# Kernel tuning notes

Measured on AMD Instinct MI355X. Metric: run time of the kernel, lower is better.

## Reference

```python
import jax, jax.numpy as jnp
import numpy as np

N = 1024      # num_waves
L = 32        # latent_dim
H = 64        # hidden_dim
EPS = 1e-6
SELF_SCALE = 0.5
INT_SCALE = 0.3


def _xavier(k, shape, gain=0.5):
    fan_out, fan_in = shape
    std = gain * np.sqrt(2.0 / (fan_in + fan_out))
    return (jax.random.normal(k, shape, jnp.float32) * std).astype(jnp.float32)


def setup_inputs() -> dict:
    key = jax.random.key(0)
    ks = jax.random.split(key, 12)
    d = {}
    d['state'] = jax.random.normal(ks[0], (N * (L + 1),), jnp.float32)
    # SelfDynamicsNetwork: L->H->H->L, tanh, xavier_normal gain=0.5, zero bias
    d['Ws1'] = _xavier(ks[1], (H, L)); d['bs1'] = jnp.zeros((H,), jnp.float32)
    d['Ws2'] = _xavier(ks[2], (H, H)); d['bs2'] = jnp.zeros((H,), jnp.float32)
    d['Ws3'] = _xavier(ks[3], (L, H)); d['bs3'] = jnp.zeros((L,), jnp.float32)
    # InteractionNetwork: 4L->H->H->L
    d['Wi1'] = _xavier(ks[4], (H, 4 * L)); d['bi1'] = jnp.zeros((H,), jnp.float32)
    d['Wi2'] = _xavier(ks[5], (H, H));     d['bi2'] = jnp.zeros((H,), jnp.float32)
    d['Wi3'] = _xavier(ks[6], (L, H));     d['bi3'] = jnp.zeros((L,), jnp.float32)
    # QuantumPhaseMixer
    d['phase_w'] = jax.random.normal(ks[7], (L,), jnp.float32) * 0.1
    d['Wc'] = _xavier(ks[8], (L, 2 * L), gain=1.0)
    d['bc'] = jnp.zeros((L,), jnp.float32)
    # per-wave aggressiveness
    d['aggr'] = jnp.ones((N,), jnp.float32) * 0.5
    return d


def reference(state, Ws1, bs1, Ws2, bs2, Ws3, bs3,
              Wi1, bi1, Wi2, bi2, Wi3, bi3,
              phase_w, Wc, bc, aggr):
    s = state.reshape(N, L + 1)
    h = s[:, :L]          # [N, L]
    phases = s[:, L]      # [N]

    def mlp(x, W1, b1, W2, b2, W3, b3):
        x = jnp.tanh(x @ W1.T + b1)
        x = jnp.tanh(x @ W2.T + b2)
        return x @ W3.T + b3

    self_term = mlp(h, Ws1, bs1, Ws2, bs2, Ws3, bs3)   # [N, L]
    dh = self_term  # prev_state is None -> estimated velocity = self_dynamics(h)

    # pairwise distance factor
    diff = h[:, None, :] - h[None, :, :]                # [N, N, L] (h_i - h_j)
    dist = jnp.linalg.norm(diff, axis=-1) + EPS         # [N, N]
    dfac = jnp.minimum(1.0 / dist, 2.0)

    # InteractionNetwork on concat([h_i, h_j, dh_i, dh_j]): split first layer
    a_i = h @ Wi1[:, :L].T + dh @ Wi1[:, 2 * L:3 * L].T           # [N, H]
    b_j = h @ Wi1[:, L:2 * L].T + dh @ Wi1[:, 3 * L:].T + bi1    # [N, H]
    x1 = jnp.tanh(a_i[:, None, :] + b_j[None, :, :])              # [N, N, H]
    x2 = jnp.tanh(x1 @ Wi2.T + bi2)                               # [N, N, H]
    k_ij = x2 @ Wi3.T + bi3                                       # [N, N, L]

    # QuantumPhaseMixer
    phase_diff = phases[:, None] - phases[None, :]                # [N, N]
    pf = jnp.cos(phase_diff[..., None] * phase_w)                 # [N, N, L]
    coh = jax.nn.sigmoid((h @ Wc[:, :L].T)[:, None, :]
                         + (h @ Wc[:, L:].T)[None, :, :] + bc)    # [N, N, L]
    quantum = pf * coh * (-diff)                                  # h_j - h_i = -diff

    agg = jax.nn.sigmoid(aggr)                                    # [N]
    inter = dfac[..., None] * k_ij * agg[:, None, None] + quantum # [N, N, L]
    mask = 1.0 - jnp.eye(N, dtype=inter.dtype)                    # skip j == i
    isum = jnp.einsum('ijl,ij->il', inter, mask)                  # sum over j

    # env is None -> speed_mults = 1, refractions = 0
    dh_dt = SELF_SCALE * self_term + INT_SCALE * isum
    dphase = 0.1 + 0.05 * jnp.sum(jnp.abs(isum), axis=-1)
    return jnp.concatenate([dh_dt, dphase[:, None]], axis=1).reshape(-1)
```

## Files before the change

### kernel.cpp

```cpp
#include <hip/hip_runtime.h>
#include <hip/hip_bf16.h>
#include <math.h>

#define NN 1024
#define LDIM 32
#define HDIM 64

#define WS_SELF 0
#define WS_AA   (WS_SELF + NN*LDIM)
#define WS_CI   (WS_AA   + NN*HDIM)
#define WS_AGG  (WS_CI   + NN*LDIM)
#define WS_BI2  (WS_AGG  + NN)
#define WS_BI3  (WS_BI2  + HDIM)
#define WS_FEND (WS_BI3  + LDIM)

#define U_BJB  0
#define U_HJB  (U_BJB + NN*HDIM)
#define U_JT   (U_HJB + NN*LDIM)
#define U_W2B  (U_JT  + NN*LDIM*4)
#define U_W3B  (U_W2B + HDIM*HDIM)
#define U_END  (U_W3B + LDIM*HDIM)

#define PK_W1  0
#define PK_W2  1024
#define PK_W3  3072
#define PK_WI1 4096
#define PK_WC  8192
#define PK_END 9216

#define K2P  2.88539008f
#define K1N  (-1.44269504f)

typedef __attribute__((ext_vector_type(8))) short bf16x8;
typedef __attribute__((ext_vector_type(4))) float f32x4;

__device__ __forceinline__ float fast_rcp(float x) { return __builtin_amdgcn_rcpf(x); }
__device__ __forceinline__ float fast_tanh(float x) {
    float e = __builtin_amdgcn_exp2f(x * K2P);
    return 1.0f - 2.0f * fast_rcp(e + 1.0f);
}
__device__ __forceinline__ float tanh_pre(float xp) {
    return 1.0f - 2.0f * fast_rcp(__builtin_amdgcn_exp2f(xp) + 1.0f);
}
__device__ __forceinline__ float fast_sigmoid(float x) {
    return fast_rcp(1.0f + __builtin_amdgcn_exp2f(x * K1N));
}
__device__ __forceinline__ float blo(unsigned int u) { union { unsigned int i; float f; } v; v.i = u << 16; return v.f; }
__device__ __forceinline__ float bhi(unsigned int u) { union { unsigned int i; float f; } v; v.i = u & 0xffff0000u; return v.f; }
__device__ __forceinline__ float bf2f(unsigned short u) { union { unsigned int i; float f; } v; v.i = ((unsigned int)u) << 16; return v.f; }
__device__ __forceinline__ unsigned short f2bf(float f) {
    __hip_bfloat16 b = __float2bfloat16(f);
    unsigned short u; __builtin_memcpy(&u, &b, 2); return u;
}
__device__ __forceinline__ unsigned int pk2(float a, float b) {
    float2 t; t.x = a; t.y = b;
    __hip_bfloat162 h = __float22bfloat162_rn(t);
    unsigned int u; __builtin_memcpy(&u, &h, 4); return u;
}

__global__ __launch_bounds__(256) void precompute(
    const float* __restrict__ state,
    const float* __restrict__ Ws1, const float* __restrict__ bs1,
    const float* __restrict__ Ws2, const float* __restrict__ bs2,
    const float* __restrict__ Ws3, const float* __restrict__ bs3,
    const float* __restrict__ Wi1, const float* __restrict__ bi1,
    const float* __restrict__ Wi2, const float* __restrict__ bi2,
    const float* __restrict__ Wi3, const float* __restrict__ bi3,
    const float* __restrict__ phw, const float* __restrict__ Wc,
    const float* __restrict__ bc,  const float* __restrict__ aggr,
    float* __restrict__ ws, unsigned short* __restrict__ wsu) {
    const int tid = threadIdx.x;
    const int w = tid >> 6, t = tid & 63;
    const int i = blockIdx.x * 4 + w;

    __shared__ unsigned int wlds[PK_END];
    __shared__ float shh[4][32], shdh[4][32], sht1[4][64], sht2[4][64];
    __shared__ float shph[4];

    {
        const float2* s1 = (const float2*)Ws1;
        #pragma unroll
        for (int r = 0; r < 4; r++) { int e = tid + r * 256; int f = e >> 4, k2 = e & 15;
            float2 v = s1[e]; wlds[PK_W1 + k2 * 64 + f] = pk2(v.x, v.y); }
        const float2* s2 = (const float2*)Ws2;
        #pragma unroll
        for (int r = 0; r < 8; r++) { int e = tid + r * 256; int f = e >> 5, k2 = e & 31;
            float2 v = s2[e]; wlds[PK_W2 + k2 * 64 + f] = pk2(v.x, v.y); }
        const float2* s3 = (const float2*)Ws3;
        #pragma unroll
        for (int r = 0; r < 4; r++) { int e = tid + r * 256; int f = e >> 5, k2 = e & 31;
            float2 v = s3[e]; wlds[PK_W3 + k2 * 32 + f] = pk2(v.x, v.y); }
        const float2* si = (const float2*)Wi1;
        #pragma unroll
        for (int r = 0; r < 16; r++) { int e = tid + r * 256; int f = e >> 6, c2 = e & 63;
            float2 v = si[e]; wlds[PK_WI1 + c2 * 64 + f] = pk2(v.x, v.y); }
        const float2* sc = (const float2*)Wc;
        #pragma unroll
        for (int r = 0; r < 4; r++) { int e = tid + r * 256; int f = e >> 5, c2 = e & 31;
            float2 v = sc[e]; wlds[PK_WC + c2 * 32 + f] = pk2(v.x, v.y); }
    }
    if (blockIdx.x == 0) {
        #pragma unroll
        for (int r = 0; r < 16; r++) { int e = tid + r * 256; wsu[U_W2B + e] = f2bf(Wi2[e] * K2P); }
        #pragma unroll
        for (int r = 0; r < 8; r++)  { int e = tid + r * 256; wsu[U_W3B + e] = f2bf(Wi3[e]); }
        if (tid < HDIM) ws[WS_BI2 + tid] = bi2[tid] * K2P;
        if (tid < LDIM) ws[WS_BI3 + tid] = bi3[tid];
    }

    float sv = (t < 33) ? state[i * 33 + t] : 0.f;
    if (t < 32) shh[w][t] = sv;
    if (t == 32) shph[w] = sv;
    if (t == 33) ws[WS_AGG + i] = fast_sigmoid(aggr[i]);
    __syncthreads();

    {
        float s = bs1[t];
        const unsigned int* W = wlds + PK_W1;
        #pragma unroll
        for (int k2 = 0; k2 < 16; k2++) {
            unsigned int p = W[k2 * 64 + t];
            s = fmaf(blo(p), shh[w][2 * k2], s);
            s = fmaf(bhi(p), shh[w][2 * k2 + 1], s);
        }
        sht1[w][t] = fast_tanh(s);
    }
    __syncthreads();
    {
        float s = bs2[t];
        const unsigned int* W = wlds + PK_W2;
        #pragma unroll
        for (int k2 = 0; k2 < 32; k2++) {
            unsigned int p = W[k2 * 64 + t];
            s = fmaf(blo(p), sht1[w][2 * k2], s);
            s = fmaf(bhi(p), sht1[w][2 * k2 + 1], s);
        }
        sht2[w][t] = fast_tanh(s);
    }
    __syncthreads();
    if (t < 32) {
        float s = bs3[t];
        const unsigned int* W = wlds + PK_W3;
        #pragma unroll
        for (int k2 = 0; k2 < 32; k2++) {
            unsigned int p = W[k2 * 32 + t];
            s = fmaf(blo(p), sht2[w][2 * k2], s);
            s = fmaf(bhi(p), sht2[w][2 * k2 + 1], s);
        }
        ws[WS_SELF + i * 32 + t] = s;
        shdh[w][t] = s;
    }
    __syncthreads();
    {
        float sa = 0.f, sb = bi1[t];
        const unsigned int* W = wlds + PK_WI1;
        #pragma unroll
        for (int k2 = 0; k2 < 16; k2++) {
            float h0 = shh[w][2 * k2], h1 = shh[w][2 * k2 + 1];
            float d0 = shdh[w][2 * k2], d1 = shdh[w][2 * k2 + 1];
            unsigned int wa  = W[k2 * 64 + t];
            unsigned int wb  = W[(16 + k2) * 64 + t];
            unsigned int wa2 = W[(32 + k2) * 64 + t];
            unsigned int wb2 = W[(48 + k2) * 64 + t];
            sa = fmaf(blo(wa), h0, sa);  sa = fmaf(bhi(wa), h1, sa);
            sb = fmaf(blo(wb), h0, sb);  sb = fmaf(bhi(wb), h1, sb);
            sa = fmaf(blo(wa2), d0, sa); sa = fmaf(bhi(wa2), d1, sa);
            sb = fmaf(blo(wb2), d0, sb); sb = fmaf(bhi(wb2), d1, sb);
        }
        ws[WS_AA + i * 64 + t]  = sa * K2P;
        wsu[U_BJB + i * 64 + t] = f2bf(sb * K2P);
    }
    if (t < 32) {
        float si = 0.f, sj = 0.f;
        const unsigned int* W = wlds + PK_WC;
        #pragma unroll
        for (int m2 = 0; m2 < 16; m2++) {
            float h0 = shh[w][2 * m2], h1 = shh[w][2 * m2 + 1];
            unsigned int wi = W[m2 * 32 + t];
            unsigned int wj = W[(16 + m2) * 32 + t];
            si = fmaf(blo(wi), h0, si); si = fmaf(bhi(wi), h1, si);
            sj = fmaf(blo(wj), h0, sj); sj = fmaf(bhi(wj), h1, sj);
        }
        ws[WS_CI + i * 32 + t] = (si + bc[t]) * K1N;
        float h = shh[w][t];
        wsu[U_HJB + i * 32 + t] = f2bf(h);
        float sc, cc;
        __sincosf(shph[w] * phw[t], &sc, &cc);
        uint2 jt; jt.x = pk2(h, sj * K1N); jt.y = pk2(cc, sc);
        *(uint2*)(wsu + U_JT + (i * 32 + t) * 4) = jt;
    }
}

__global__ __launch_bounds__(256) void pair_kernel(
    const float* __restrict__ ws, const unsigned short* __restrict__ wsu,
    float* __restrict__ out) {
    const int i    = blockIdx.x;
    const int tid  = threadIdx.x;
    const int w    = tid >> 6;
    const int lane = tid & 63;
    const int q    = lane >> 4;
    const int m    = lane & 15;
    const int jw   = w * 16;
    const int sub  = lane & 3;

    __shared__ unsigned short W2ls[64 * 72];
    __shared__ unsigned short W3ls[32 * 72];
    __shared__ unsigned short x2ls[4 * 2 * 16 * 72];
    __shared__ float aLS[64];
    __shared__ float redT[4][32], redU[4][32], redV[4][32];
    __shared__ float sfw[4];

    if (tid < 64) aLS[tid] = ws[WS_AA + i * 64 + tid];
    {
        int row = tid >> 2, c = (tid & 3) * 16;
        const uint4* s2 = (const uint4*)(wsu + U_W2B + row * 64 + c);
        uint4 d0 = s2[0], d1 = s2[1];
        uint4* dd = (uint4*)(&W2ls[row * 72 + c]);
        dd[0] = d0; dd[1] = d1;
        if (row < 32) {
            const uint4* s3 = (const uint4*)(wsu + U_W3B + row * 64 + c);
            uint4 e0 = s3[0], e1 = s3[1];
            uint4* d3 = (uint4*)(&W3ls[row * 72 + c]);
            d3[0] = e0; d3[1] = e1;
        }
    }
    float hi8[8];
    {
        uint4 hv4 = *(const uint4*)(wsu + U_HJB + i * 32 + sub * 8);
        unsigned int hd[4] = {hv4.x, hv4.y, hv4.z, hv4.w};
        #pragma unroll
        for (int e = 0; e < 4; e++) { hi8[2 * e] = blo(hd[e]); hi8[2 * e + 1] = bhi(hd[e]); }
    }
    f32x4 b2q[4];
    #pragma unroll
    for (int nb = 0; nb < 4; nb++) {
        float4 bv = *(const float4*)(ws + WS_BI2 + nb * 16 + q * 4);
        b2q[nb][0] = bv.x; b2q[nb][1] = bv.y; b2q[nb][2] = bv.z; b2q[nb][3] = bv.w;
    }
    float hiv[2], cibv[2];
    #pragma unroll
    for (int lb = 0; lb < 2; lb++) {
        int l = lb * 16 + m;
        hiv[lb]  = bf2f(wsu[U_HJB + i * 32 + l]);
        cibv[lb] = ws[WS_CI + i * 32 + l];
    }
    const float aggi = ws[WS_AGG + i];
    const float sub0 = (sub == 0) ? 1.0f : 0.0f;

    const unsigned short* hp = wsu + U_HJB + (jw + (lane >> 2)) * 32 + sub * 8;
    const unsigned short* bp = wsu + U_BJB + (jw + m) * 64 + q * 8;
    const unsigned short* jp = wsu + U_JT + ((jw + q * 4) * 32 + m) * 4;

    uint4 hvA = *(const uint4*)hp;
    uint4 b0A = *(const uint4*)bp;
    uint4 b1A = *(const uint4*)(bp + 32);
    uint4 hvB, b0B, b1B;
    __syncthreads();

    f32x4 accK[2];
    #pragma unroll
    for (int lb = 0; lb < 2; lb++) { accK[lb][0]=0.f; accK[lb][1]=0.f; accK[lb][2]=0.f; accK[lb][3]=0.f; }
    float aU[2] = {0.f, 0.f}, aV[2] = {0.f, 0.f};
    float sumfac = 0.f;

    unsigned short* xb0 = &x2ls[w * 2 * 1152];
    unsigned short* xb1 = xb0 + 1152;

    auto stageB = [&](const unsigned short* xb) {
        bf16x8 x2f[2];
        #pragma unroll
        for (int s = 0; s < 2; s++)
            x2f[s] = *(const bf16x8*)(&xb[m * 72 + s * 32 + q * 8]);
        #pragma unroll
        for (int lb = 0; lb < 2; lb++) {
            #pragma unroll
            for (int s = 0; s < 2; s++) {
                bf16x8 w3f = *(const bf16x8*)(&W3ls[(lb * 16 + m) * 72 + s * 32 + q * 8]);
                accK[lb] = __builtin_amdgcn_mfma_f32_16x16x32_bf16(x2f[s], w3f, accK[lb], 0, 0, 0);
            }
        }
    };

    auto body = [&](int T, uint4 hvc, uint4 b0c, uint4 b1c,
                    uint4& hvn, uint4& b0n, uint4& b1n,
                    unsigned short* xcur, const unsigned short* xprev) {
        hp += 2048; bp += 4096;
        hvn = *(const uint4*)hp;
        b0n = *(const uint4*)bp;
        b1n = *(const uint4*)(bp + 32);
        uint2 jt[8];
        #pragma unroll
        for (int r = 0; r < 4; r++) {
            jt[r]     = *(const uint2*)(jp + r * 128);
            jt[4 + r] = *(const uint2*)(jp + 64 + r * 128);
        }
        jp += 8192;

        if (T > 0) stageB(xprev);

        float facm;
        {
            unsigned int hd[4] = {hvc.x, hvc.y, hvc.z, hvc.w};
            float s = 0.f;
            #pragma unroll
            for (int e = 0; e < 4; e++) {
                float d0 = hi8[2 * e]     - blo(hd[e]);
                float d1 = hi8[2 * e + 1] - bhi(hd[e]);
                s = fmaf(d0, d0, s); s = fmaf(d1, d1, s);
            }
            s += __shfl_xor(s, 1); s += __shfl_xor(s, 2);
            int jj = T * 64 + jw + (lane >> 2);
            float facown = fminf(__builtin_amdgcn_rsqf(s), 2.0f) * aggi;
            facown = (jj == i) ? 0.0f : facown;
            sumfac = fmaf(sub0, facown, sumfac);
            facm = __shfl(facown, 4 * m);
        }
        const float fm2 = -2.0f * facm;

        bf16x8 afr[2];
        {
            unsigned int bd[8] = {b0c.x, b0c.y, b0c.z, b0c.w, b1c.x, b1c.y, b1c.z, b1c.w};
            #pragma unroll
            for (int s = 0; s < 2; s++) {
                union { uint4 u4; bf16x8 v; } pkd;
                #pragma unroll
                for (int e = 0; e < 4; e++) {
                    const float* ab = &aLS[s * 32 + q * 8 + 2 * e];
                    float x0 = tanh_pre(ab[0] + blo(bd[s * 4 + e]));
                    float x1 = tanh_pre(ab[1] + bhi(bd[s * 4 + e]));
                    ((unsigned int*)&pkd.u4)[e] = pk2(x0, x1);
                }
                afr[s] = pkd.v;
            }
        }

        f32x4 accA[4];
        #pragma unroll
        for (int nb = 0; nb < 4; nb++) {
            f32x4 acc = b2q[nb];
            #pragma unroll
            for (int s = 0; s < 2; s++) {
                bf16x8 w2f = *(const bf16x8*)(&W2ls[(nb * 16 + m) * 72 + s * 32 + q * 8]);
                acc = __builtin_amdgcn_mfma_f32_16x16x32_bf16(w2f, afr[s], acc, 0, 0, 0);
            }
            accA[nb] = acc;
        }
        #pragma unroll
        for (int nb = 0; nb < 4; nb++) {
            float r0 = fast_rcp(__builtin_amdgcn_exp2f(accA[nb][0]) + 1.0f);
            float r1 = fast_rcp(__builtin_amdgcn_exp2f(accA[nb][1]) + 1.0f);
            float r2 = fast_rcp(__builtin_amdgcn_exp2f(accA[nb][2]) + 1.0f);
            float r3 = fast_rcp(__builtin_amdgcn_exp2f(accA[nb][3]) + 1.0f);
            float t0 = fmaf(fm2, r0, facm), t1 = fmaf(fm2, r1, facm);
            float t2 = fmaf(fm2, r2, facm), t3 = fmaf(fm2, r3, facm);
            uint2 pk; pk.x = pk2(t0, t1); pk.y = pk2(t2, t3);
            *(uint2*)(&xcur[m * 72 + nb * 16 + q * 4]) = pk;
        }

        #pragma unroll
        for (int lb = 0; lb < 2; lb++) {
            float u = 0.f, v = 0.f;
            #pragma unroll
            for (int r = 0; r < 4; r++) {
                uint2 jv = jt[lb * 4 + r];
                float hj = blo(jv.x), cj = bhi(jv.x);
                float pjc = blo(jv.y), pjs = bhi(jv.y);
                float coh = fast_rcp(1.0f + __builtin_amdgcn_exp2f(cibv[lb] + cj));
                float cd  = coh * (hiv[lb] - hj);
                u = fmaf(cd, pjc, u);
                v = fmaf(cd, pjs, v);
            }
            aU[lb] += u; aV[lb] += v;
        }
    };

    #pragma unroll 1
    for (int T = 0; T < 16; T += 2) {
        body(T,     hvA, b0A, b1A, hvB, b0B, b1B, xb0, xb1);
        body(T + 1, hvB, b0B, b1B, hvA, b0A, b1A, xb1, xb0);
    }
    stageB(xb1);

    float T1[2];
    #pragma unroll
    for (int lb = 0; lb < 2; lb++) {
        T1[lb] = (accK[lb][0] + accK[lb][1]) + (accK[lb][2] + accK[lb][3]);
        T1[lb] += __shfl_xor(T1[lb], 16); T1[lb] += __shfl_xor(T1[lb], 32);
        aU[lb] += __shfl_xor(aU[lb], 16); aU[lb] += __shfl_xor(aU[lb], 32);
        aV[lb] += __shfl_xor(aV[lb], 16); aV[lb] += __shfl_xor(aV[lb], 32);
    }
    sumfac += __shfl_xor(sumfac, 1);  sumfac += __shfl_xor(sumfac, 2);
    sumfac += __shfl_xor(sumfac, 4);  sumfac += __shfl_xor(sumfac, 8);
    sumfac += __shfl_xor(sumfac, 16); sumfac += __shfl_xor(sumfac, 32);
    if (lane < 16) {
        redT[w][m] = T1[0];      redT[w][16 + m] = T1[1];
        redU[w][m] = aU[0];      redU[w][16 + m] = aU[1];
        redV[w][m] = aV[0];      redV[w][16 + m] = aV[1];
    }
    if (lane == 0) sfw[w] = sumfac;
    __syncthreads();
    if (tid < 32) {
        int l = tid;
        float t1 = (redT[0][l] + redT[1][l]) + (redT[2][l] + redT[3][l]);
        float uu = (redU[0][l] + redU[1][l]) + (redU[2][l] + redU[3][l]);
        float vv = (redV[0][l] + redV[1][l]) + (redV[2][l] + redV[3][l]);
        float sf = (sfw[0] + sfw[1]) + (sfw[2] + sfw[3]);
        uint2 jti = *(const uint2*)(wsu + U_JT + (i * 32 + l) * 4);
        float pic = blo(jti.y), pis = bhi(jti.y);
        float isum = t1 + sf * ws[WS_BI3 + l] - (pic * uu + pis * vv);
        out[i * 33 + l] = 0.5f * ws[WS_SELF + i * 32 + l] + 0.3f * isum;
        redT[0][l] = fabsf(isum);
    }
    __syncthreads();
    if (tid == 0) {
        float s = 0.f;
        #pragma unroll
        for (int l = 0; l < 32; l++) s += redT[0][l];
        out[i * 33 + 32] = 0.1f + 0.05f * s;
    }
}

extern "C" void kernel_launch(void* const* d_in, const int* in_sizes, int n_in,
                              void* d_out, int out_size, void* d_ws, size_t ws_size,
                              hipStream_t stream) {
    const float* state   = (const float*)d_in[0];
    const float* Ws1     = (const float*)d_in[1];
    const float* bs1     = (const float*)d_in[2];
    const float* Ws2     = (const float*)d_in[3];
    const float* bs2     = (const float*)d_in[4];
    const float* Ws3     = (const float*)d_in[5];
    const float* bs3     = (const float*)d_in[6];
    const float* Wi1     = (const float*)d_in[7];
    const float* bi1     = (const float*)d_in[8];
    const float* Wi2     = (const float*)d_in[9];
    const float* bi2     = (const float*)d_in[10];
    const float* Wi3     = (const float*)d_in[11];
    const float* bi3     = (const float*)d_in[12];
    const float* phase_w = (const float*)d_in[13];
    const float* Wc      = (const float*)d_in[14];
    const float* bc      = (const float*)d_in[15];
    const float* aggr    = (const float*)d_in[16];

    float* ws = (float*)d_ws;
    unsigned short* wsu = (unsigned short*)(ws + WS_FEND);
    float* out = (float*)d_out;

    precompute<<<256, 256, 0, stream>>>(state, Ws1, bs1, Ws2, bs2, Ws3, bs3,
                                        Wi1, bi1, Wi2, bi2, Wi3, bi3,
                                        phase_w, Wc, bc, aggr, ws, wsu);
    pair_kernel<<<NN, 256, 0, stream>>>(ws, wsu, out);
}
```

Measured before the change: 149.8 us.

## Pack pair-kernel math into float2 ops with shared reciprocals and repacked JT layout

Rewrites the pair kernel's tanh, sigmoid and distance math on two-wide float vectors so the compiler can emit packed FP32 instructions, and computes two reciprocals from one rcp of the product. The phase/coherence table is repacked so lanes m and m+16 share one 16-byte load, and the a_i values move from LDS into registers. The final abs-sum uses wave shuffles instead of a barrier plus serial loop, and launch bounds request 4 blocks per CU. Sharing one rcp across two values risks overflow or precision loss when the exp terms are large, and holding a_i in registers adds register pressure.

```diff
diff --git a/kernel.cpp b/kernel.cpp
--- a/kernel.cpp
+++ b/kernel.cpp
@@ -33,14 +33,12 @@
 
 typedef __attribute__((ext_vector_type(8))) short bf16x8;
 typedef __attribute__((ext_vector_type(4))) float f32x4;
+typedef __attribute__((ext_vector_type(2))) float v2f;
 
 __device__ __forceinline__ float fast_rcp(float x) { return __builtin_amdgcn_rcpf(x); }
 __device__ __forceinline__ float fast_tanh(float x) {
     float e = __builtin_amdgcn_exp2f(x * K2P);
     return 1.0f - 2.0f * fast_rcp(e + 1.0f);
-}
-__device__ __forceinline__ float tanh_pre(float xp) {
-    return 1.0f - 2.0f * fast_rcp(__builtin_amdgcn_exp2f(xp) + 1.0f);
 }
 __device__ __forceinline__ float fast_sigmoid(float x) {
     return fast_rcp(1.0f + __builtin_amdgcn_exp2f(x * K1N));
@@ -56,6 +54,15 @@
     float2 t; t.x = a; t.y = b;
     __hip_bfloat162 h = __float22bfloat162_rn(t);
     unsigned int u; __builtin_memcpy(&u, &h, 4); return u;
+}
+
+__device__ __forceinline__ v2f tanh2_pre(v2f xp) {
+    v2f e; e.x = __builtin_amdgcn_exp2f(xp.x); e.y = __builtin_amdgcn_exp2f(xp.y);
+    v2f d = e + 1.0f;
+    float rr = fast_rcp(d.x * d.y);
+    v2f sw; sw.x = d.y; sw.y = d.x;
+    v2f r = sw * rr;
+    return 1.0f - 2.0f * r;
 }
 
 __global__ __launch_bounds__(256) void precompute(
@@ -171,27 +178,36 @@
         wsu[U_BJB + i * 64 + t] = f2bf(sb * K2P);
     }
     if (t < 32) {
-        float si = 0.f, sj = 0.f;
+        float si2 = 0.f, sj = 0.f;
         const unsigned int* W = wlds + PK_WC;
         #pragma unroll
         for (int m2 = 0; m2 < 16; m2++) {
             float h0 = shh[w][2 * m2], h1 = shh[w][2 * m2 + 1];
             unsigned int wi = W[m2 * 32 + t];
             unsigned int wj = W[(16 + m2) * 32 + t];
-            si = fmaf(blo(wi), h0, si); si = fmaf(bhi(wi), h1, si);
-            sj = fmaf(blo(wj), h0, sj); sj = fmaf(bhi(wj), h1, sj);
-        }
-        ws[WS_CI + i * 32 + t] = (si + bc[t]) * K1N;
+            si2 = fmaf(blo(wi), h0, si2); si2 = fmaf(bhi(wi), h1, si2);
+            sj  = fmaf(blo(wj), h0, sj);  sj  = fmaf(bhi(wj), h1, sj);
+        }
+        ws[WS_CI + i * 32 + t] = (si2 + bc[t]) * K1N;
         float h = shh[w][t];
         wsu[U_HJB + i * 32 + t] = f2bf(h);
-        float sc, cc;
-        __sincosf(shph[w] * phw[t], &sc, &cc);
-        uint2 jt; jt.x = pk2(h, sj * K1N); jt.y = pk2(cc, sc);
-        *(uint2*)(wsu + U_JT + (i * 32 + t) * 4) = jt;
-    }
-}
-
-__global__ __launch_bounds__(256) void pair_kernel(
+        float cjn = sj * K1N;
+        float sc_, cc_;
+        __sincosf(shph[w] * phw[t], &sc_, &cc_);
+        int p = (t & 15) + 16;
+        float h_p  = __shfl(h,   p);
+        float c_p  = __shfl(cjn, p);
+        float cc_p = __shfl(cc_, p);
+        float sc_p = __shfl(sc_, p);
+        if (t < 16) {
+            uint4 o; o.x = pk2(h, h_p); o.y = pk2(cjn, c_p);
+            o.z = pk2(cc_, cc_p); o.w = pk2(sc_, sc_p);
+            *(uint4*)(wsu + U_JT + (i * 16 + t) * 8) = o;
+        }
+    }
+}
+
+__global__ __launch_bounds__(256, 4) void pair_kernel(
     const float* __restrict__ ws, const unsigned short* __restrict__ wsu,
     float* __restrict__ out) {
     const int i    = blockIdx.x;
@@ -206,11 +222,9 @@
     __shared__ unsigned short W2ls[64 * 72];
     __shared__ unsigned short W3ls[32 * 72];
     __shared__ unsigned short x2ls[4 * 2 * 16 * 72];
-    __shared__ float aLS[64];
     __shared__ float redT[4][32], redU[4][32], redV[4][32];
     __shared__ float sfw[4];
 
-    if (tid < 64) aLS[tid] = ws[WS_AA + i * 64 + tid];
     {
         int row = tid >> 2, c = (tid & 3) * 16;
         const uint4* s2 = (const uint4*)(wsu + U_W2B + row * 64 + c);
@@ -224,12 +238,12 @@
             d3[0] = e0; d3[1] = e1;
         }
     }
-    float hi8[8];
+    v2f hi2[4];
     {
         uint4 hv4 = *(const uint4*)(wsu + U_HJB + i * 32 + sub * 8);
         unsigned int hd[4] = {hv4.x, hv4.y, hv4.z, hv4.w};
         #pragma unroll
-        for (int e = 0; e < 4; e++) { hi8[2 * e] = blo(hd[e]); hi8[2 * e + 1] = bhi(hd[e]); }
+        for (int e = 0; e < 4; e++) { hi2[e].x = blo(hd[e]); hi2[e].y = bhi(hd[e]); }
     }
     f32x4 b2q[4];
     #pragma unroll
@@ -237,19 +251,28 @@
         float4 bv = *(const float4*)(ws + WS_BI2 + nb * 16 + q * 4);
         b2q[nb][0] = bv.x; b2q[nb][1] = bv.y; b2q[nb][2] = bv.z; b2q[nb][3] = bv.w;
     }
-    float hiv[2], cibv[2];
-    #pragma unroll
-    for (int lb = 0; lb < 2; lb++) {
-        int l = lb * 16 + m;
-        hiv[lb]  = bf2f(wsu[U_HJB + i * 32 + l]);
-        cibv[lb] = ws[WS_CI + i * 32 + l];
-    }
+    v2f av2[8];
+    {
+        const float* ap = ws + WS_AA + i * 64 + q * 8;
+        #pragma unroll
+        for (int s = 0; s < 2; s++) {
+            float4 lo = *(const float4*)(ap + s * 32);
+            float4 hi = *(const float4*)(ap + s * 32 + 4);
+            av2[s * 4 + 0].x = lo.x; av2[s * 4 + 0].y = lo.y;
+            av2[s * 4 + 1].x = lo.z; av2[s * 4 + 1].y = lo.w;
+            av2[s * 4 + 2].x = hi.x; av2[s * 4 + 2].y = hi.y;
+            av2[s * 4 + 3].x = hi.z; av2[s * 4 + 3].y = hi.w;
+        }
+    }
+    v2f hiv2, cib2;
+    hiv2.x = bf2f(wsu[U_HJB + i * 32 + m]);      hiv2.y = bf2f(wsu[U_HJB + i * 32 + 16 + m]);
+    cib2.x = ws[WS_CI + i * 32 + m];             cib2.y = ws[WS_CI + i * 32 + 16 + m];
     const float aggi = ws[WS_AGG + i];
     const float sub0 = (sub == 0) ? 1.0f : 0.0f;
 
     const unsigned short* hp = wsu + U_HJB + (jw + (lane >> 2)) * 32 + sub * 8;
     const unsigned short* bp = wsu + U_BJB + (jw + m) * 64 + q * 8;
-    const unsigned short* jp = wsu + U_JT + ((jw + q * 4) * 32 + m) * 4;
+    const unsigned short* jp = wsu + U_JT + ((jw + q * 4) * 16 + m) * 8;
 
     uint4 hvA = *(const uint4*)hp;
     uint4 b0A = *(const uint4*)bp;
@@ -260,7 +283,8 @@
     f32x4 accK[2];
     #pragma unroll
     for (int lb = 0; lb < 2; lb++) { accK[lb][0]=0.f; accK[lb][1]=0.f; accK[lb][2]=0.f; accK[lb][3]=0.f; }
-    float aU[2] = {0.f, 0.f}, aV[2] = {0.f, 0.f};
+    v2f u2; u2.x = 0.f; u2.y = 0.f;
+    v2f vv2; vv2.x = 0.f; vv2.y = 0.f;
     float sumfac = 0.f;
 
     unsigned short* xb0 = &x2ls[w * 2 * 1152];
@@ -288,31 +312,25 @@
         hvn = *(const uint4*)hp;
         b0n = *(const uint4*)bp;
         b1n = *(const uint4*)(bp + 32);
-        uint2 jt[8];
-        #pragma unroll
-        for (int r = 0; r < 4; r++) {
-            jt[r]     = *(const uint2*)(jp + r * 128);
-            jt[4 + r] = *(const uint2*)(jp + 64 + r * 128);
-        }
-        jp += 8192;
 
         if (T > 0) stageB(xprev);
 
         float facm;
         {
             unsigned int hd[4] = {hvc.x, hvc.y, hvc.z, hvc.w};
-            float s = 0.f;
+            v2f s2v; s2v.x = 0.f; s2v.y = 0.f;
             #pragma unroll
             for (int e = 0; e < 4; e++) {
-                float d0 = hi8[2 * e]     - blo(hd[e]);
-                float d1 = hi8[2 * e + 1] - bhi(hd[e]);
-                s = fmaf(d0, d0, s); s = fmaf(d1, d1, s);
+                v2f hj; hj.x = blo(hd[e]); hj.y = bhi(hd[e]);
+                v2f d = hi2[e] - hj;
+                s2v += d * d;
             }
+            float s = s2v.x + s2v.y;
             s += __shfl_xor(s, 1); s += __shfl_xor(s, 2);
             int jj = T * 64 + jw + (lane >> 2);
             float facown = fminf(__builtin_amdgcn_rsqf(s), 2.0f) * aggi;
             facown = (jj == i) ? 0.0f : facown;
-            sumfac = fmaf(sub0, facown, sumfac);
+            sumfac = fmaf(sub0, facown, facown * 0.0f + sumfac);
             facm = __shfl(facown, 4 * m);
         }
         const float fm2 = -2.0f * facm;
@@ -325,14 +343,19 @@
                 union { uint4 u4; bf16x8 v; } pkd;
                 #pragma unroll
                 for (int e = 0; e < 4; e++) {
-                    const float* ab = &aLS[s * 32 + q * 8 + 2 * e];
-                    float x0 = tanh_pre(ab[0] + blo(bd[s * 4 + e]));
-                    float x1 = tanh_pre(ab[1] + bhi(bd[s * 4 + e]));
-                    ((unsigned int*)&pkd.u4)[e] = pk2(x0, x1);
+                    unsigned int bw = bd[s * 4 + e];
+                    v2f b2; b2.x = blo(bw); b2.y = bhi(bw);
+                    v2f t2 = tanh2_pre(av2[s * 4 + e] + b2);
+                    ((unsigned int*)&pkd.u4)[e] = pk2(t2.x, t2.y);
                 }
                 afr[s] = pkd.v;
             }
         }
+
+        uint4 jt4[4];
+        #pragma unroll
+        for (int r = 0; r < 4; r++) jt4[r] = *(const uint4*)(jp + r * 128);
+        jp += 8192;
 
         f32x4 accA[4];
         #pragma unroll
@@ -347,30 +370,35 @@
         }
         #pragma unroll
         for (int nb = 0; nb < 4; nb++) {
-            float r0 = fast_rcp(__builtin_amdgcn_exp2f(accA[nb][0]) + 1.0f);
-            float r1 = fast_rcp(__builtin_amdgcn_exp2f(accA[nb][1]) + 1.0f);
-            float r2 = fast_rcp(__builtin_amdgcn_exp2f(accA[nb][2]) + 1.0f);
-            float r3 = fast_rcp(__builtin_amdgcn_exp2f(accA[nb][3]) + 1.0f);
-            float t0 = fmaf(fm2, r0, facm), t1 = fmaf(fm2, r1, facm);
-            float t2 = fmaf(fm2, r2, facm), t3 = fmaf(fm2, r3, facm);
-            uint2 pk; pk.x = pk2(t0, t1); pk.y = pk2(t2, t3);
+            v2f eA; eA.x = __builtin_amdgcn_exp2f(accA[nb][0]); eA.y = __builtin_amdgcn_exp2f(accA[nb][1]);
+            v2f eB; eB.x = __builtin_amdgcn_exp2f(accA[nb][2]); eB.y = __builtin_amdgcn_exp2f(accA[nb][3]);
+            v2f dA = eA + 1.0f, dB = eB + 1.0f;
+            float rA = fast_rcp(dA.x * dA.y), rB = fast_rcp(dB.x * dB.y);
+            v2f swA; swA.x = dA.y; swA.y = dA.x;
+            v2f swB; swB.x = dB.y; swB.y = dB.x;
+            v2f rvA = swA * rA, rvB = swB * rB;
+            v2f tA = rvA * fm2 + facm;
+            v2f tB = rvB * fm2 + facm;
+            uint2 pk; pk.x = pk2(tA.x, tA.y); pk.y = pk2(tB.x, tB.y);
             *(uint2*)(&xcur[m * 72 + nb * 16 + q * 4]) = pk;
         }
 
         #pragma unroll
-        for (int lb = 0; lb < 2; lb++) {
-            float u = 0.f, v = 0.f;
-            #pragma unroll
-            for (int r = 0; r < 4; r++) {
-                uint2 jv = jt[lb * 4 + r];
-                float hj = blo(jv.x), cj = bhi(jv.x);
-                float pjc = blo(jv.y), pjs = bhi(jv.y);
-                float coh = fast_rcp(1.0f + __builtin_amdgcn_exp2f(cibv[lb] + cj));
-                float cd  = coh * (hiv[lb] - hj);
-                u = fmaf(cd, pjc, u);
-                v = fmaf(cd, pjs, v);
-            }
-            aU[lb] += u; aV[lb] += v;
+        for (int r = 0; r < 4; r++) {
+            uint4 jv = jt4[r];
+            v2f hj2; hj2.x = blo(jv.x); hj2.y = bhi(jv.x);
+            v2f cj2; cj2.x = blo(jv.y); cj2.y = bhi(jv.y);
+            v2f pc2; pc2.x = blo(jv.z); pc2.y = bhi(jv.z);
+            v2f ps2; ps2.x = blo(jv.w); ps2.y = bhi(jv.w);
+            v2f arg = cib2 + cj2;
+            v2f ee; ee.x = __builtin_amdgcn_exp2f(arg.x); ee.y = __builtin_amdgcn_exp2f(arg.y);
+            v2f dd = ee + 1.0f;
+            float rr = fast_rcp(dd.x * dd.y);
+            v2f swd; swd.x = dd.y; swd.y = dd.x;
+            v2f coh = swd * rr;
+            v2f cd = coh * (hiv2 - hj2);
+            u2  += cd * pc2;
+            vv2 += cd * ps2;
         }
     };
 
@@ -382,6 +410,8 @@
     stageB(xb1);
 
     float T1[2];
+    float aU[2] = {u2.x, u2.y};
+    float aV[2] = {vv2.x, vv2.y};
     #pragma unroll
     for (int lb = 0; lb < 2; lb++) {
         T1[lb] = (accK[lb][0] + accK[lb][1]) + (accK[lb][2] + accK[lb][3]);
@@ -403,20 +433,19 @@
         int l = tid;
         float t1 = (redT[0][l] + redT[1][l]) + (redT[2][l] + redT[3][l]);
         float uu = (redU[0][l] + redU[1][l]) + (redU[2][l] + redU[3][l]);
-        float vv = (redV[0][l] + redV[1][l]) + (redV[2][l] + redV[3][l]);
+        float vvv = (redV[0][l] + redV[1][l]) + (redV[2][l] + redV[3][l]);
         float sf = (sfw[0] + sfw[1]) + (sfw[2] + sfw[3]);
-        uint2 jti = *(const uint2*)(wsu + U_JT + (i * 32 + l) * 4);
-        float pic = blo(jti.y), pis = bhi(jti.y);
-        float isum = t1 + sf * ws[WS_BI3 + l] - (pic * uu + pis * vv);
+        int mm = l & 15;
+        uint2 jti = *(const uint2*)(wsu + U_JT + (i * 16 + mm) * 8 + 4);
+        float pic = (l < 16) ? blo(jti.x) : bhi(jti.x);
+        float pis = (l < 16) ? blo(jti.y) : bhi(jti.y);
+        float isum = t1 + sf * ws[WS_BI3 + l] - (pic * uu + pis * vvv);
         out[i * 33 + l] = 0.5f * ws[WS_SELF + i * 32 + l] + 0.3f * isum;
-        redT[0][l] = fabsf(isum);
-    }
-    __syncthreads();
-    if (tid == 0) {
-        float s = 0.f;
-        #pragma unroll
-        for (int l = 0; l < 32; l++) s += redT[0][l];
-        out[i * 33 + 32] = 0.1f + 0.05f * s;
+        float ab = fabsf(isum);
+        ab += __shfl_xor(ab, 1); ab += __shfl_xor(ab, 2);
+        ab += __shfl_xor(ab, 4); ab += __shfl_xor(ab, 8);
+        ab += __shfl_xor(ab, 16);
+        if (tid == 0) out[i * 33 + 32] = 0.1f + 0.05f * ab;
     }
 }
 
```

After: 249.2 us. 66.3% more time.
